# Optimization experiments

Measured on AMD Instinct MI355X. Metric: run time of the kernel, lower is better.

The kernel has to match this reference:

```python
import jax, jax.numpy as jnp
import numpy as np

B, T, C, H = 4, 2048, 1024, 16
NEG = -1e9  # masked-fill value (finite to keep grads clean)


def setup_inputs() -> dict:
    key = jax.random.key(0)
    ks = jax.random.split(key, 5)
    s = 1.0 / np.sqrt(C)  # keep logits O(1) like trained linear layers
    return {
        "x": jax.random.normal(ks[0], (B, T, C), dtype=jnp.float32),
        "wq": jax.random.normal(ks[1], (C, C), dtype=jnp.float32) * s,
        "bq": jnp.zeros((C,), dtype=jnp.float32),
        "wk": jax.random.normal(ks[2], (C, C), dtype=jnp.float32) * s,
        "bk": jnp.zeros((C,), dtype=jnp.float32),
        "wv": jax.random.normal(ks[3], (C, C), dtype=jnp.float32) * s,
        "bv": jnp.zeros((C,), dtype=jnp.float32),
        "wo": jax.random.normal(ks[4], (C, C), dtype=jnp.float32) * s,
        "bo": jnp.zeros((C,), dtype=jnp.float32),
    }


def _split_heads(y):
    # [B,T,C] -> [B,H,T,hd]
    b, t, c = y.shape
    return y.reshape(b, t, H, c // H).transpose(0, 2, 1, 3)


def reference(x, wq, bq, wk, bk, wv, bv, wo, bo):
    b, t, c = x.shape
    scale = (c // H) ** (-0.5)
    q = _split_heads(x @ wq.T + bq)  # [B,H,T,hd]
    k = _split_heads(x @ wk.T + bk)
    v = _split_heads(x @ wv.T + bv)
    att = jnp.einsum("bhqd,bhkd->bhqk", q, k) * scale  # [B,H,T,T]
    causal = jnp.tril(jnp.ones((t, t), dtype=bool))
    att = jnp.where(causal[None, None], att, NEG)
    att = jax.nn.softmax(att, axis=-1)  # dropout is identity in eval mode
    y = jnp.einsum("bhqk,bhkd->bhqd", att, v)
    y = y.transpose(0, 2, 1, 3).reshape(b, t, c)
    return y @ wo.T + bo
```

## Files before the change

### kernel.cpp

```cpp
#include <hip/hip_runtime.h>


#define B_ 4
#define T_ 2048
#define C_ 1024
#define H_ 16
#define M_ 8192

typedef unsigned short u16;
typedef __bf16 bf16x8 __attribute__((ext_vector_type(8)));
typedef float f32x4 __attribute__((ext_vector_type(4)));

static __device__ __forceinline__ u16 f2bf(float f) {
  unsigned int u = __float_as_uint(f);
  u += 0x7fffu + ((u >> 16) & 1u);
  return (u16)(u >> 16);
}

static __device__ __forceinline__ void async16(const void* g, void* l) {
  __builtin_amdgcn_global_load_lds(
      (const __attribute__((address_space(1))) unsigned int*)g,
      (__attribute__((address_space(3))) unsigned int*)l, 16, 0, 0);
}

#if __has_builtin(__builtin_amdgcn_exp2f)
#define EXP2F(x) __builtin_amdgcn_exp2f(x)
#else
#define EXP2F(x) exp2f(x)
#endif

static __device__ __forceinline__ f32x4 mfma32(bf16x8 a, bf16x8 b, f32x4 c) {
  return __builtin_amdgcn_mfma_f32_16x16x32_bf16(a, b, c, 0, 0, 0);
}

static __device__ __forceinline__ unsigned int cvtpk(float lo, float hi) {
  unsigned int r;
  asm("v_cvt_pk_bf16_f32 %0, %1, %2" : "=v"(r) : "v"(lo), "v"(hi));
  return r;
}

#define FENCE() asm volatile("" ::: "memory")

__global__ __launch_bounds__(256) void cvt_all(const float* __restrict__ x,
                                               const float* __restrict__ w0,
                                               const float* __restrict__ w1,
                                               const float* __restrict__ w2,
                                               const float* __restrict__ w3,
                                               u16* __restrict__ xb,
                                               u16* __restrict__ wb,
                                               float s0) {
  const int NX = M_ * C_ / 4, NW = C_ * C_ / 4;
  int i = blockIdx.x * 256 + threadIdx.x;
  const float* src;
  u16* dst;
  int idx;
  float s = 1.f;
  if (i < NX) {
    src = x; dst = xb; idx = i;
  } else {
    int j = i - NX;
    int w = j / NW;
    idx = j - w * NW;
    src = (w == 0) ? w0 : (w == 1) ? w1 : (w == 2) ? w2 : w3;
    dst = wb + (size_t)w * C_ * C_;
    if (w == 0) s = s0;
  }
  float4 f = ((const float4*)src)[idx];
  ushort4 o;
  o.x = f2bf(f.x * s); o.y = f2bf(f.y * s); o.z = f2bf(f.z * s); o.w = f2bf(f.w * s);
  ((ushort4*)dst)[idx] = o;
}

__global__ __launch_bounds__(512, 1) void gemm_qkv(const u16* __restrict__ A,
                                                   const u16* __restrict__ W,
                                                   const float* __restrict__ bq,
                                                   const float* __restrict__ bk,
                                                   const float* __restrict__ bv,
                                                   float qscale,
                                                   u16* __restrict__ outqk,
                                                   u16* __restrict__ vtb) {
  __shared__ __align__(16) union {
    u16 buf[3][24576];
    u16 Cu[256 * 136];
    u16 Ct[128 * 272];
  } sm;
  const int tid = threadIdx.x, lane = tid & 63, wave = tid >> 6;
  const int quad = lane >> 4, l16 = lane & 15;
  const int wm = wave >> 1, wn = wave & 1;
  const int bid = blockIdx.x;
  const int xcd = bid & 7, idx = bid >> 3;
  const int cq = idx >> 2;
  const int row0 = (xcd * 4 + (idx & 3)) * 256;
  const int sel = cq >> 3, colw = cq & 7;
  const int col0 = colw * 128;
  const u16* Bt = W + (size_t)sel * C_ * C_;
  const float* bias = sel == 0 ? bq : (sel == 1 ? bk : bv);
  const float bscale = sel == 0 ? qscale : 1.f;

  const u16* aptr[4];
  const u16* bptr[2];
#pragma unroll
  for (int it = 0; it < 4; it++) {
    int c = it * 512 + tid, r = c >> 3, g = (c & 7) ^ (r & 7);
    aptr[it] = A + (size_t)(row0 + r) * C_ + g * 8;
  }
#pragma unroll
  for (int it = 0; it < 2; it++) {
    int c = it * 512 + tid, r = c >> 3, g = (c & 7) ^ (r & 7);
    bptr[it] = Bt + (size_t)(col0 + r) * C_ + g * 8;
  }

  auto STAGE = [&](int t, int pp) {
    const int k0 = t * 64;
    u16* lA = sm.buf[pp];
    u16* lB = sm.buf[pp] + 16384;
#pragma unroll
    for (int it = 0; it < 4; it++)
      async16(aptr[it] + k0, lA + (size_t)(it * 512 + wave * 64) * 8);
#pragma unroll
    for (int it = 0; it < 2; it++)
      async16(bptr[it] + k0, lB + (size_t)(it * 512 + wave * 64) * 8);
  };

  f32x4 zero = {0.f, 0.f, 0.f, 0.f};
  f32x4 acc[4][4];
#pragma unroll
  for (int i = 0; i < 4; i++)
#pragma unroll
    for (int j = 0; j < 4; j++) acc[i][j] = zero;

  STAGE(0, 0);
  STAGE(1, 1);

  int p = 0, p2 = 2;
#pragma unroll 1
  for (int u = 0; u < 16; ++u) {
    FENCE();
    __builtin_amdgcn_s_barrier();
    FENCE();
    if (u < 14) STAGE(u + 2, p2);
    if (u < 14) {
      asm volatile("s_waitcnt vmcnt(12)" ::: "memory");
    } else if (u < 15) {
      asm volatile("s_waitcnt vmcnt(6)" ::: "memory");
    } else {
      asm volatile("s_waitcnt vmcnt(0)" ::: "memory");
    }
    FENCE();
    __builtin_amdgcn_s_barrier();
    FENCE();

    const u16* As = sm.buf[p];
    const u16* Bs = sm.buf[p] + 16384;
    bf16x8 bfr[4][2];
#pragma unroll
    for (int j = 0; j < 4; j++) {
      int rn = wn * 64 + 16 * j + l16;
#pragma unroll
      for (int kk = 0; kk < 2; kk++)
        bfr[j][kk] =
            *(const bf16x8*)(Bs + rn * 64 + (((kk * 4 + quad) ^ (rn & 7)) * 8));
    }
    {
      bf16x8 a2[2][2];
#pragma unroll
      for (int i = 0; i < 2; i++) {
        int rm = wm * 64 + 16 * i + l16;
#pragma unroll
        for (int kk = 0; kk < 2; kk++)
          a2[i][kk] =
              *(const bf16x8*)(As + rm * 64 + (((kk * 4 + quad) ^ (rm & 7)) * 8));
      }
      __builtin_amdgcn_s_setprio(1);
#pragma unroll
      for (int i = 0; i < 2; i++)
#pragma unroll
        for (int j = 0; j < 4; j++) {
          acc[i][j] = mfma32(a2[i][0], bfr[j][0], acc[i][j]);
          acc[i][j] = mfma32(a2[i][1], bfr[j][1], acc[i][j]);
        }
      __builtin_amdgcn_s_setprio(0);
    }
    FENCE();
    __builtin_amdgcn_s_barrier();
    FENCE();
    {
      bf16x8 a2[2][2];
#pragma unroll
      for (int i = 0; i < 2; i++) {
        int rm = wm * 64 + 16 * (i + 2) + l16;
#pragma unroll
        for (int kk = 0; kk < 2; kk++)
          a2[i][kk] =
              *(const bf16x8*)(As + rm * 64 + (((kk * 4 + quad) ^ (rm & 7)) * 8));
      }
      __builtin_amdgcn_s_setprio(1);
#pragma unroll
      for (int i = 0; i < 2; i++)
#pragma unroll
        for (int j = 0; j < 4; j++) {
          acc[i + 2][j] = mfma32(a2[i][0], bfr[j][0], acc[i + 2][j]);
          acc[i + 2][j] = mfma32(a2[i][1], bfr[j][1], acc[i + 2][j]);
        }
      __builtin_amdgcn_s_setprio(0);
    }
    asm volatile("s_waitcnt lgkmcnt(0)" ::: "memory");
    p = (p == 2) ? 0 : p + 1;
    p2 = (p2 == 2) ? 0 : p2 + 1;
  }
  __syncthreads();

  float bj[4];
#pragma unroll
  for (int j = 0; j < 4; j++) bj[j] = bias[col0 + wn * 64 + 16 * j + l16] * bscale;

  if (sel == 2) {
#pragma unroll
    for (int i = 0; i < 4; i++)
#pragma unroll
      for (int j = 0; j < 4; j++) {
        int lc = wn * 64 + 16 * j + l16;
        int rt = wm * 64 + 16 * i + quad * 4;
        union { u16 s[4]; uint2 u; } w;
#pragma unroll
        for (int r = 0; r < 4; r++) w.s[r] = f2bf(acc[i][j][r] + bj[j]);
        *(uint2*)(sm.Ct + (size_t)lc * 272 + rt) = w.u;
      }
    __syncthreads();
    const int bb = row0 >> 11, t0 = row0 & 2047;
#pragma unroll
    for (int c2 = 0; c2 < 8; c2++) {
      int c = c2 * 512 + tid;
      int nr = c >> 5, ch = c & 31;
      bf16x8 v = *(const bf16x8*)(sm.Ct + (size_t)nr * 272 + ch * 8);
      int gn = col0 + nr, d = gn & 63, hh = gn >> 6;
      *(bf16x8*)(vtb + ((size_t)((bb * 16 + hh) * 64 + d)) * T_ + t0 + ch * 8) = v;
    }
  } else {
#pragma unroll
    for (int i = 0; i < 4; i++)
#pragma unroll
      for (int j = 0; j < 4; j++) {
        int lc = wn * 64 + 16 * j + l16;
        int rt = wm * 64 + 16 * i + quad * 4;
#pragma unroll
        for (int r = 0; r < 4; r++)
          sm.Cu[(size_t)(rt + r) * 136 + lc] = f2bf(acc[i][j][r] + bj[j]);
      }
    __syncthreads();
    u16* dst = outqk + (size_t)sel * M_ * C_;
#pragma unroll
    for (int c2 = 0; c2 < 8; c2++) {
      int c = c2 * 512 + tid;
      int rw = c >> 4, ch = c & 15;
      bf16x8 v = *(const bf16x8*)(sm.Cu + (size_t)rw * 136 + ch * 8);
      *(bf16x8*)(dst + (size_t)(row0 + rw) * C_ + col0 + ch * 8) = v;
    }
  }
}

__global__ __launch_bounds__(512, 1) void gemm_o(const u16* __restrict__ A,
                                                 const u16* __restrict__ Bt,
                                                 const float* __restrict__ bias,
                                                 float* __restrict__ outf) {
  __shared__ __align__(16) union {
    u16 buf[3][24576];
    float Cf[256 * 132];
  } sm;
  const int tid = threadIdx.x, lane = tid & 63, wave = tid >> 6;
  const int quad = lane >> 4, l16 = lane & 15;
  const int wm = wave >> 1, wn = wave & 1;
  const int bid = blockIdx.x;
  const int xcd = bid & 7, idx = bid >> 3;
  const int row0 = (xcd * 4 + (idx & 3)) * 256;
  const int col0 = (idx >> 2) * 128;

  const u16* aptr[4];
  const u16* bptr[2];
#pragma unroll
  for (int it = 0; it < 4; it++) {
    int c = it * 512 + tid, r = c >> 3, g = (c & 7) ^ (r & 7);
    aptr[it] = A + (size_t)(row0 + r) * C_ + g * 8;
  }
#pragma unroll
  for (int it = 0; it < 2; it++) {
    int c = it * 512 + tid, r = c >> 3, g = (c & 7) ^ (r & 7);
    bptr[it] = Bt + (size_t)(col0 + r) * C_ + g * 8;
  }

  auto STAGE = [&](int t, int pp) {
    const int k0 = t * 64;
    u16* lA = sm.buf[pp];
    u16* lB = sm.buf[pp] + 16384;
#pragma unroll
    for (int it = 0; it < 4; it++)
      async16(aptr[it] + k0, lA + (size_t)(it * 512 + wave * 64) * 8);
#pragma unroll
    for (int it = 0; it < 2; it++)
      async16(bptr[it] + k0, lB + (size_t)(it * 512 + wave * 64) * 8);
  };

  f32x4 zero = {0.f, 0.f, 0.f, 0.f};
  f32x4 acc[4][4];
#pragma unroll
  for (int i = 0; i < 4; i++)
#pragma unroll
    for (int j = 0; j < 4; j++) acc[i][j] = zero;

  STAGE(0, 0);
  STAGE(1, 1);

  int p = 0, p2 = 2;
#pragma unroll 1
  for (int u = 0; u < 16; ++u) {
    FENCE();
    __builtin_amdgcn_s_barrier();
    FENCE();
    if (u < 14) STAGE(u + 2, p2);
    if (u < 14) {
      asm volatile("s_waitcnt vmcnt(12)" ::: "memory");
    } else if (u < 15) {
      asm volatile("s_waitcnt vmcnt(6)" ::: "memory");
    } else {
      asm volatile("s_waitcnt vmcnt(0)" ::: "memory");
    }
    FENCE();
    __builtin_amdgcn_s_barrier();
    FENCE();

    const u16* As = sm.buf[p];
    const u16* Bs = sm.buf[p] + 16384;
    bf16x8 bfr[4][2];
#pragma unroll
    for (int j = 0; j < 4; j++) {
      int rn = wn * 64 + 16 * j + l16;
#pragma unroll
      for (int kk = 0; kk < 2; kk++)
        bfr[j][kk] =
            *(const bf16x8*)(Bs + rn * 64 + (((kk * 4 + quad) ^ (rn & 7)) * 8));
    }
    {
      bf16x8 a2[2][2];
#pragma unroll
      for (int i = 0; i < 2; i++) {
        int rm = wm * 64 + 16 * i + l16;
#pragma unroll
        for (int kk = 0; kk < 2; kk++)
          a2[i][kk] =
              *(const bf16x8*)(As + rm * 64 + (((kk * 4 + quad) ^ (rm & 7)) * 8));
      }
      __builtin_amdgcn_s_setprio(1);
#pragma unroll
      for (int i = 0; i < 2; i++)
#pragma unroll
        for (int j = 0; j < 4; j++) {
          acc[i][j] = mfma32(a2[i][0], bfr[j][0], acc[i][j]);
          acc[i][j] = mfma32(a2[i][1], bfr[j][1], acc[i][j]);
        }
      __builtin_amdgcn_s_setprio(0);
    }
    FENCE();
    __builtin_amdgcn_s_barrier();
    FENCE();
    {
      bf16x8 a2[2][2];
#pragma unroll
      for (int i = 0; i < 2; i++) {
        int rm = wm * 64 + 16 * (i + 2) + l16;
#pragma unroll
        for (int kk = 0; kk < 2; kk++)
          a2[i][kk] =
              *(const bf16x8*)(As + rm * 64 + (((kk * 4 + quad) ^ (rm & 7)) * 8));
      }
      __builtin_amdgcn_s_setprio(1);
#pragma unroll
      for (int i = 0; i < 2; i++)
#pragma unroll
        for (int j = 0; j < 4; j++) {
          acc[i + 2][j] = mfma32(a2[i][0], bfr[j][0], acc[i + 2][j]);
          acc[i + 2][j] = mfma32(a2[i][1], bfr[j][1], acc[i + 2][j]);
        }
      __builtin_amdgcn_s_setprio(0);
    }
    asm volatile("s_waitcnt lgkmcnt(0)" ::: "memory");
    p = (p == 2) ? 0 : p + 1;
    p2 = (p2 == 2) ? 0 : p2 + 1;
  }
  __syncthreads();

  float bj[4];
#pragma unroll
  for (int j = 0; j < 4; j++) bj[j] = bias[col0 + wn * 64 + 16 * j + l16];

#pragma unroll
  for (int i = 0; i < 4; i++)
#pragma unroll
    for (int j = 0; j < 4; j++) {
      int lc = wn * 64 + 16 * j + l16;
      int rt = wm * 64 + 16 * i + quad * 4;
#pragma unroll
      for (int r = 0; r < 4; r++)
        sm.Cf[(size_t)(rt + r) * 132 + lc] = acc[i][j][r] + bj[j];
    }
  __syncthreads();
#pragma unroll
  for (int c2 = 0; c2 < 16; c2++) {
    int c = c2 * 512 + tid;
    int rw = c >> 5, c4 = c & 31;
    float4 v = *(const float4*)(sm.Cf + (size_t)rw * 132 + c4 * 4);
    *(float4*)(outf + (size_t)(row0 + rw) * C_ + col0 + c4 * 4) = v;
  }
}

__global__ __launch_bounds__(256) void attn(const u16* __restrict__ q,
                                            const u16* __restrict__ k,
                                            const u16* __restrict__ vt,
                                            u16* __restrict__ y) {
  __shared__ __align__(16) u16 Ksm[2][128 * 64];
  __shared__ __align__(16) u16 Vsm[2][2][64 * 64];
  const int tid = threadIdx.x, lane = tid & 63, wave = tid >> 6;
  const int quad = lane >> 4, l16 = lane & 15;
  static const int qperm[16] = {15, 14, 11, 10, 12, 13, 8, 9, 3, 2, 7, 6, 0, 1, 4, 5};
  const int bh = blockIdx.x;
  const int qt = qperm[blockIdx.y];
  const int b = bh >> 4, h = bh & 15;

  const int S0 = ((lane & 15) + ((lane >> 4) & 1) * 32) * 4;
  const int S1 = S0 + 64;
  const bool hi32 = (lane & 32) != 0;

  bf16x8 qf[2][2];
#pragma unroll
  for (int m = 0; m < 2; m++) {
    const u16* qp =
        q + (size_t)(b * T_ + qt * 128 + wave * 32 + m * 16 + l16) * C_ + h * 64;
#pragma unroll
    for (int ks = 0; ks < 2; ks++)
      qf[m][ks] = *(const bf16x8*)(qp + ks * 32 + quad * 8);
  }

  f32x4 zero = {0.f, 0.f, 0.f, 0.f};
  f32x4 o[2][4];
  float lps[2] = {0.f, 0.f};
#pragma unroll
  for (int m = 0; m < 2; m++)
#pragma unroll
    for (int dt = 0; dt < 4; dt++) o[m][dt] = zero;

  const u16* kp[4];
  const u16* vp[4];
#pragma unroll
  for (int i = 0; i < 4; i++) {
    int c = i * 256 + tid;
    int r = c >> 3, lc = (c & 7) ^ (r & 7);
    kp[i] = k + (size_t)(b * T_ + r) * C_ + h * 64 + lc * 8;
  }
#pragma unroll
  for (int s = 0; s < 2; s++)
#pragma unroll
    for (int i = 0; i < 2; i++) {
      int c = i * 256 + tid;
      int r = c >> 3, lc = (c & 7) ^ (r & 7);
      vp[s * 2 + i] = vt + (size_t)(bh * 64 + r) * T_ + 64 * s + lc * 8;
    }

  auto stageKV = [&](int jt, int ss) {
    const size_t koff = (size_t)jt * 128 * C_;
    const int voff = jt * 128;
#pragma unroll
    for (int i = 0; i < 4; i++)
      async16(kp[i] + koff, Ksm[ss] + (size_t)(i * 256 + wave * 64) * 8);
#pragma unroll
    for (int s = 0; s < 2; s++)
#pragma unroll
      for (int i = 0; i < 2; i++)
        async16(vp[s * 2 + i] + voff, Vsm[ss][s] + (size_t)(i * 256 + wave * 64) * 8);
  };

  const int qrow = wave * 32 + l16;

  stageKV(0, 0);

#pragma unroll 1
  for (int jt = 0; jt <= qt; ++jt) {
    const int cs = jt & 1;
    __syncthreads();
    if (jt < qt) stageKV(jt + 1, cs ^ 1);

    const bool diag = (jt == qt);
#pragma unroll
    for (int hh = 0; hh < 2; ++hh) {
      if (diag && (2 * wave + 2 - 4 * hh) <= 0) continue;
      unsigned int pk[2][4][2];
#pragma unroll
      for (int n = 0; n < 4; ++n) {
        int rk = hh * 64 + n * 16 + l16;
        bf16x8 kf0 = *(const bf16x8*)(Ksm[cs] + rk * 64 + ((quad ^ (rk & 7)) * 8));
        bf16x8 kf1 = *(const bf16x8*)(Ksm[cs] + rk * 64 + (((4 + quad) ^ (rk & 7)) * 8));
#pragma unroll
        for (int m = 0; m < 2; ++m) {
          int nlim = diag ? (2 * wave + m + 1 - 4 * hh) : 4;
          float e[4];
          if (n < nlim) {
            f32x4 s = mfma32(kf0, qf[m][0], zero);
            s = mfma32(kf1, qf[m][1], s);
#pragma unroll
            for (int r = 0; r < 4; r++) e[r] = EXP2F(s[r]);
            if (diag) {
              int rmax = qrow + m * 16 - hh * 64 - n * 16 - quad * 4;
#pragma unroll
              for (int r = 0; r < 4; r++)
                if (r > rmax) e[r] = 0.f;
            }
            lps[m] += (e[0] + e[1]) + (e[2] + e[3]);
          } else {
#pragma unroll
            for (int r = 0; r < 4; r++) e[r] = 0.f;
          }
          pk[m][n][0] = cvtpk(e[0], e[1]);
          pk[m][n][1] = cvtpk(e[2], e[3]);
        }
      }
      bf16x8 pa[2][2];
#pragma unroll
      for (int m = 0; m < 2; ++m)
#pragma unroll
        for (int ks = 0; ks < 2; ++ks) {
          union { unsigned int u[4]; bf16x8 v; } uu;
#pragma unroll
          for (int c = 0; c < 2; ++c) {
            int x = (int)pk[m][2 * ks][c];
            int yv = (int)pk[m][2 * ks + 1][c];
            int bx0 = __builtin_amdgcn_ds_bpermute(S0, x);
            int by0 = __builtin_amdgcn_ds_bpermute(S0, yv);
            int bx1 = __builtin_amdgcn_ds_bpermute(S1, x);
            int by1 = __builtin_amdgcn_ds_bpermute(S1, yv);
            uu.u[c] = (unsigned int)(hi32 ? by0 : bx0);
            uu.u[2 + c] = (unsigned int)(hi32 ? by1 : bx1);
          }
          pa[m][ks] = uu.v;
        }
#pragma unroll
      for (int dt = 0; dt < 4; ++dt) {
        int rv = dt * 16 + l16;
        bf16x8 vf0 = *(const bf16x8*)(Vsm[cs][hh] + rv * 64 + ((quad ^ (rv & 7)) * 8));
        bf16x8 vf1 =
            *(const bf16x8*)(Vsm[cs][hh] + rv * 64 + (((4 + quad) ^ (rv & 7)) * 8));
#pragma unroll
        for (int m = 0; m < 2; m++) {
          o[m][dt] = mfma32(pa[m][0], vf0, o[m][dt]);
          o[m][dt] = mfma32(pa[m][1], vf1, o[m][dt]);
        }
      }
    }
  }

  float linv[2];
#pragma unroll
  for (int m = 0; m < 2; m++) {
    float v = lps[m];
    v += __shfl_xor(v, 16);
    v += __shfl_xor(v, 32);
    linv[m] = 1.f / v;
  }

#pragma unroll
  for (int m = 0; m < 2; m++)
#pragma unroll
    for (int r = 0; r < 4; r++) {
      float il = __shfl(linv[m], quad * 4 + r);
      int grow = b * T_ + qt * 128 + wave * 32 + m * 16 + quad * 4 + r;
#pragma unroll
      for (int dt = 0; dt < 4; dt++)
        y[(size_t)grow * C_ + h * 64 + dt * 16 + l16] = f2bf(o[m][dt][r] * il);
    }
}

extern "C" void kernel_launch(void* const* d_in, const int* in_sizes, int n_in,
                              void* d_out, int out_size, void* d_ws, size_t ws_size,
                              hipStream_t stream) {
  const float* x  = (const float*)d_in[0];
  const float* wq = (const float*)d_in[1];
  const float* bq = (const float*)d_in[2];
  const float* wk = (const float*)d_in[3];
  const float* bk = (const float*)d_in[4];
  const float* wv = (const float*)d_in[5];
  const float* bv = (const float*)d_in[6];
  const float* wo = (const float*)d_in[7];
  const float* bo = (const float*)d_in[8];
  float* out = (float*)d_out;

  const float QSCALE = 0.125f * 1.4426950408889634f;

  u16* xb  = (u16*)d_ws;
  u16* wqb = xb  + (size_t)M_ * C_;
  u16* wob = wqb + 3 * (size_t)C_ * C_;
  u16* qb  = wob + (size_t)C_ * C_;
  u16* kb  = qb  + (size_t)M_ * C_;
  u16* vtb = kb  + (size_t)M_ * C_;
  u16* yb  = xb;

  const int NCVT = (M_ * C_ + 4 * C_ * C_) / 4 / 256;
  cvt_all<<<NCVT, 256, 0, stream>>>(x, wq, wk, wv, wo, xb, wqb, QSCALE);

  gemm_qkv<<<768, 512, 0, stream>>>(xb, wqb, bq, bk, bv, QSCALE, qb, vtb);

  attn<<<dim3(B_ * H_, 16), 256, 0, stream>>>(qb, kb, vtb, yb);

  gemm_o<<<256, 512, 0, stream>>>(yb, wob, bo, out);
}
```

Measured before the change: 269.0 us.

## Split attention work across 8 waves with 16 query rows each

```diff
diff --git a/kernel.cpp b/kernel.cpp
--- a/kernel.cpp
+++ b/kernel.cpp
@@ -412,7 +412,7 @@
   }
 }
 
-__global__ __launch_bounds__(256) void attn(const u16* __restrict__ q,
+__global__ __launch_bounds__(512) void attn(const u16* __restrict__ q,
                                             const u16* __restrict__ k,
                                             const u16* __restrict__ vt,
                                             u16* __restrict__ y) {
@@ -420,64 +420,57 @@
   __shared__ __align__(16) u16 Vsm[2][2][64 * 64];
   const int tid = threadIdx.x, lane = tid & 63, wave = tid >> 6;
   const int quad = lane >> 4, l16 = lane & 15;
-  static const int qperm[16] = {15, 14, 11, 10, 12, 13, 8, 9, 3, 2, 7, 6, 0, 1, 4, 5};
+  const int rb = wave;
   const int bh = blockIdx.x;
-  const int qt = qperm[blockIdx.y];
+  const int qt = 15 - blockIdx.y;
   const int b = bh >> 4, h = bh & 15;
 
   const int S0 = ((lane & 15) + ((lane >> 4) & 1) * 32) * 4;
   const int S1 = S0 + 64;
   const bool hi32 = (lane & 32) != 0;
 
-  bf16x8 qf[2][2];
-#pragma unroll
-  for (int m = 0; m < 2; m++) {
+  bf16x8 qf[2];
+  {
     const u16* qp =
-        q + (size_t)(b * T_ + qt * 128 + wave * 32 + m * 16 + l16) * C_ + h * 64;
+        q + (size_t)(b * T_ + qt * 128 + rb * 16 + l16) * C_ + h * 64;
 #pragma unroll
     for (int ks = 0; ks < 2; ks++)
-      qf[m][ks] = *(const bf16x8*)(qp + ks * 32 + quad * 8);
+      qf[ks] = *(const bf16x8*)(qp + ks * 32 + quad * 8);
   }
 
   f32x4 zero = {0.f, 0.f, 0.f, 0.f};
-  f32x4 o[2][4];
-  float lps[2] = {0.f, 0.f};
-#pragma unroll
-  for (int m = 0; m < 2; m++)
-#pragma unroll
-    for (int dt = 0; dt < 4; dt++) o[m][dt] = zero;
-
-  const u16* kp[4];
-  const u16* vp[4];
-#pragma unroll
-  for (int i = 0; i < 4; i++) {
-    int c = i * 256 + tid;
+  f32x4 o[4];
+  float lps = 0.f;
+#pragma unroll
+  for (int dt = 0; dt < 4; dt++) o[dt] = zero;
+
+  const u16* kp[2];
+#pragma unroll
+  for (int i = 0; i < 2; i++) {
+    int c = i * 512 + tid;
     int r = c >> 3, lc = (c & 7) ^ (r & 7);
     kp[i] = k + (size_t)(b * T_ + r) * C_ + h * 64 + lc * 8;
   }
-#pragma unroll
-  for (int s = 0; s < 2; s++)
-#pragma unroll
-    for (int i = 0; i < 2; i++) {
-      int c = i * 256 + tid;
-      int r = c >> 3, lc = (c & 7) ^ (r & 7);
-      vp[s * 2 + i] = vt + (size_t)(bh * 64 + r) * T_ + 64 * s + lc * 8;
-    }
+  const u16* vp[2];
+#pragma unroll
+  for (int s = 0; s < 2; s++) {
+    int c = tid;
+    int r = c >> 3, lc = (c & 7) ^ (r & 7);
+    vp[s] = vt + (size_t)(bh * 64 + r) * T_ + 64 * s + lc * 8;
+  }
 
   auto stageKV = [&](int jt, int ss) {
-    const size_t koff = (size_t)jt * 128 * C_;
-    const int voff = jt * 128;
-#pragma unroll
-    for (int i = 0; i < 4; i++)
-      async16(kp[i] + koff, Ksm[ss] + (size_t)(i * 256 + wave * 64) * 8);
+    const size_t ko = (size_t)jt * 128 * C_;
+    const int vo = jt * 128;
+#pragma unroll
+    for (int i = 0; i < 2; i++)
+      async16(kp[i] + ko, Ksm[ss] + (size_t)(i * 512 + wave * 64) * 8);
 #pragma unroll
     for (int s = 0; s < 2; s++)
-#pragma unroll
-      for (int i = 0; i < 2; i++)
-        async16(vp[s * 2 + i] + voff, Vsm[ss][s] + (size_t)(i * 256 + wave * 64) * 8);
+      async16(vp[s] + vo, Vsm[ss][s] + (size_t)(wave * 64) * 8);
   };
 
-  const int qrow = wave * 32 + l16;
+  const int qrow = rb * 16 + l16;
 
   stageKV(0, 0);
 
@@ -490,90 +483,81 @@
     const bool diag = (jt == qt);
 #pragma unroll
     for (int hh = 0; hh < 2; ++hh) {
-      if (diag && (2 * wave + 2 - 4 * hh) <= 0) continue;
-      unsigned int pk[2][4][2];
+      if (diag && (rb + 1 - 4 * hh) <= 0) continue;
+      unsigned int pk[4][2];
+      const int nlim = diag ? (rb + 1 - 4 * hh) : 4;
 #pragma unroll
       for (int n = 0; n < 4; ++n) {
-        int rk = hh * 64 + n * 16 + l16;
-        bf16x8 kf0 = *(const bf16x8*)(Ksm[cs] + rk * 64 + ((quad ^ (rk & 7)) * 8));
-        bf16x8 kf1 = *(const bf16x8*)(Ksm[cs] + rk * 64 + (((4 + quad) ^ (rk & 7)) * 8));
-#pragma unroll
-        for (int m = 0; m < 2; ++m) {
-          int nlim = diag ? (2 * wave + m + 1 - 4 * hh) : 4;
-          float e[4];
-          if (n < nlim) {
-            f32x4 s = mfma32(kf0, qf[m][0], zero);
-            s = mfma32(kf1, qf[m][1], s);
-#pragma unroll
-            for (int r = 0; r < 4; r++) e[r] = EXP2F(s[r]);
-            if (diag) {
-              int rmax = qrow + m * 16 - hh * 64 - n * 16 - quad * 4;
-#pragma unroll
-              for (int r = 0; r < 4; r++)
-                if (r > rmax) e[r] = 0.f;
-            }
-            lps[m] += (e[0] + e[1]) + (e[2] + e[3]);
-          } else {
-#pragma unroll
-            for (int r = 0; r < 4; r++) e[r] = 0.f;
+        float e[4];
+        if (n < nlim) {
+          int rk = hh * 64 + n * 16 + l16;
+          bf16x8 kf0 = *(const bf16x8*)(Ksm[cs] + rk * 64 + ((quad ^ (rk & 7)) * 8));
+          bf16x8 kf1 =
+              *(const bf16x8*)(Ksm[cs] + rk * 64 + (((4 + quad) ^ (rk & 7)) * 8));
+          f32x4 s = mfma32(kf0, qf[0], zero);
+          s = mfma32(kf1, qf[1], s);
+#pragma unroll
+          for (int r = 0; r < 4; r++) e[r] = EXP2F(s[r]);
+          if (diag) {
+            int rmax = qrow - hh * 64 - n * 16 - quad * 4;
+#pragma unroll
+            for (int r = 0; r < 4; r++)
+              if (r > rmax) e[r] = 0.f;
           }
-          pk[m][n][0] = cvtpk(e[0], e[1]);
-          pk[m][n][1] = cvtpk(e[2], e[3]);
+          lps += (e[0] + e[1]) + (e[2] + e[3]);
+        } else {
+#pragma unroll
+          for (int r = 0; r < 4; r++) e[r] = 0.f;
         }
-      }
-      bf16x8 pa[2][2];
-#pragma unroll
-      for (int m = 0; m < 2; ++m)
-#pragma unroll
-        for (int ks = 0; ks < 2; ++ks) {
-          union { unsigned int u[4]; bf16x8 v; } uu;
-#pragma unroll
-          for (int c = 0; c < 2; ++c) {
-            int x = (int)pk[m][2 * ks][c];
-            int yv = (int)pk[m][2 * ks + 1][c];
-            int bx0 = __builtin_amdgcn_ds_bpermute(S0, x);
-            int by0 = __builtin_amdgcn_ds_bpermute(S0, yv);
-            int bx1 = __builtin_amdgcn_ds_bpermute(S1, x);
-            int by1 = __builtin_amdgcn_ds_bpermute(S1, yv);
-            uu.u[c] = (unsigned int)(hi32 ? by0 : bx0);
-            uu.u[2 + c] = (unsigned int)(hi32 ? by1 : bx1);
-          }
-          pa[m][ks] = uu.v;
+        pk[n][0] = cvtpk(e[0], e[1]);
+        pk[n][1] = cvtpk(e[2], e[3]);
+      }
+      bf16x8 pa[2];
+#pragma unroll
+      for (int ks = 0; ks < 2; ++ks) {
+        union { unsigned int u[4]; bf16x8 v; } uu;
+#pragma unroll
+        for (int c = 0; c < 2; ++c) {
+          int x = (int)pk[2 * ks][c];
+          int yv = (int)pk[2 * ks + 1][c];
+          int bx0 = __builtin_amdgcn_ds_bpermute(S0, x);
+          int by0 = __builtin_amdgcn_ds_bpermute(S0, yv);
+          int bx1 = __builtin_amdgcn_ds_bpermute(S1, x);
+          int by1 = __builtin_amdgcn_ds_bpermute(S1, yv);
+          uu.u[c] = (unsigned int)(hi32 ? by0 : bx0);
+          uu.u[2 + c] = (unsigned int)(hi32 ? by1 : bx1);
         }
+        pa[ks] = uu.v;
+      }
 #pragma unroll
       for (int dt = 0; dt < 4; ++dt) {
         int rv = dt * 16 + l16;
-        bf16x8 vf0 = *(const bf16x8*)(Vsm[cs][hh] + rv * 64 + ((quad ^ (rv & 7)) * 8));
+        bf16x8 vf0 =
+            *(const bf16x8*)(Vsm[cs][hh] + rv * 64 + ((quad ^ (rv & 7)) * 8));
         bf16x8 vf1 =
             *(const bf16x8*)(Vsm[cs][hh] + rv * 64 + (((4 + quad) ^ (rv & 7)) * 8));
-#pragma unroll
-        for (int m = 0; m < 2; m++) {
-          o[m][dt] = mfma32(pa[m][0], vf0, o[m][dt]);
-          o[m][dt] = mfma32(pa[m][1], vf1, o[m][dt]);
-        }
-      }
-    }
-  }
-
-  float linv[2];
-#pragma unroll
-  for (int m = 0; m < 2; m++) {
-    float v = lps[m];
+        o[dt] = mfma32(pa[0], vf0, o[dt]);
+        o[dt] = mfma32(pa[1], vf1, o[dt]);
+      }
+    }
+  }
+
+  float linv;
+  {
+    float v = lps;
     v += __shfl_xor(v, 16);
     v += __shfl_xor(v, 32);
-    linv[m] = 1.f / v;
-  }
-
-#pragma unroll
-  for (int m = 0; m < 2; m++)
-#pragma unroll
-    for (int r = 0; r < 4; r++) {
-      float il = __shfl(linv[m], quad * 4 + r);
-      int grow = b * T_ + qt * 128 + wave * 32 + m * 16 + quad * 4 + r;
-#pragma unroll
-      for (int dt = 0; dt < 4; dt++)
-        y[(size_t)grow * C_ + h * 64 + dt * 16 + l16] = f2bf(o[m][dt][r] * il);
-    }
+    linv = 1.f / v;
+  }
+
+#pragma unroll
+  for (int r = 0; r < 4; r++) {
+    float il = __shfl(linv, quad * 4 + r);
+    int grow = b * T_ + qt * 128 + rb * 16 + quad * 4 + r;
+#pragma unroll
+    for (int dt = 0; dt < 4; dt++)
+      y[(size_t)grow * C_ + h * 64 + dt * 16 + l16] = f2bf(o[dt][r] * il);
+  }
 }
 
 extern "C" void kernel_launch(void* const* d_in, const int* in_sizes, int n_in,
@@ -605,7 +589,7 @@
 
   gemm_qkv<<<768, 512, 0, stream>>>(xb, wqb, bq, bk, bv, QSCALE, qb, vtb);
 
-  attn<<<dim3(B_ * H_, 16), 256, 0, stream>>>(qb, kb, vtb, yb);
+  attn<<<dim3(B_ * H_, 16), 512, 0, stream>>>(qb, kb, vtb, yb);
 
   gemm_o<<<256, 512, 0, stream>>>(yb, wob, bo, out);
 }
```

Result: faster. 257.6 us (-4.2%).
